# Kernel tuning notes

Hardware: AMD Instinct MI355X
Metric: run time of the kernel (lower is better)

## Reference

```python
import jax, jax.numpy as jnp
import numpy as np

GRID_SHAPE = (256, 256)  # SOM lattice dims -> M = 65536 nodes, ndim = 2
D = 32                   # input feature dim
B = 2048                 # batch size


def _make_grid_flat():
    # tf.meshgrid(indexing='ij') stacked on last axis, flattened to [1, M, ndim]
    mesh = np.stack(np.meshgrid(*[np.arange(s) for s in GRID_SHAPE], indexing='ij'), axis=-1)
    g = mesh.reshape(1, -1, len(GRID_SHAPE)).astype(np.float32)
    # faithful to source: per-axis mean (reduce_mean axis=1), GLOBAL std (reduce_std, no axis)
    g = (g - g.mean(axis=1, keepdims=True)) / g.std()
    return jnp.asarray(g)


def setup_inputs() -> dict:
    key = jax.random.key(0)
    k1, k2 = jax.random.split(key)
    grid_flat = _make_grid_flat()                                  # [1, M, 2]
    M = grid_flat.shape[1]
    w = jax.random.normal(k1, (1, M, D), dtype=jnp.float32)        # codebook (non-trainable in source)
    x = jax.random.normal(k2, (B, D), dtype=jnp.float32)
    return {"x": x, "grid_flat": grid_flat, "w": w}


def reference(x, grid_flat, w):
    # squared L2 distance from each input to every codebook vector.
    # computed here without materializing the [B, M, D] broadcast.
    wm = w[0]  # [M, D]
    d2 = (jnp.sum(x * x, axis=1, keepdims=True)
          - 2.0 * (x @ wm.T)
          + jnp.sum(wm * wm, axis=1)[None, :])  # [B, M]
    # source: top_k(-|d2|, k=1); d2 >= 0 so abs is identity, kept for fidelity
    _, idx = jax.lax.top_k(-jnp.abs(d2), 1)  # idx: [B, 1]
    bmu = grid_flat[0][idx[:, 0]]            # gather winning grid coords -> [B, 2]
    return bmu
```

## Files before the change

kernel.cpp:

```cpp
#include <hip/hip_runtime.h>
#include <stdint.h>

#define D       32
#define B       2048
#define M       65536
#define STRIPS  1024
#define CHUNKS  4
#define CHCOLS  (B / CHUNKS)
#define NTILES  (CHCOLS / 16)
#define SGROUPS 32
#define SPERG   (STRIPS / SGROUPS)

typedef _Float16 half8  __attribute__((ext_vector_type(8)));
typedef _Float16 half4v __attribute__((ext_vector_type(4)));
typedef float    floatx4 __attribute__((ext_vector_type(4)));


__device__ __forceinline__ uint32_t f32_sortable(float f) {
    uint32_t u = __float_as_uint(f);
    u ^= (uint32_t)((int32_t)u >> 31) | 0x80000000u;
    return u;
}

__global__ void som_prep_kernel(const float* __restrict__ x,
                                _Float16* __restrict__ xh,
                                _Float16* __restrict__ xl) {
    int i = (blockIdx.x * 256 + threadIdx.x) * 4;
    float4 v = *(const float4*)(x + i);
    half4v h, l;
    h[0] = (_Float16)v.x; l[0] = (_Float16)(v.x - (float)h[0]);
    h[1] = (_Float16)v.y; l[1] = (_Float16)(v.y - (float)h[1]);
    h[2] = (_Float16)v.z; l[2] = (_Float16)(v.z - (float)h[2]);
    h[3] = (_Float16)v.w; l[3] = (_Float16)(v.w - (float)h[3]);
    *(half4v*)(xh + i) = h;
    *(half4v*)(xl + i) = l;
}

__global__ __launch_bounds__(256, 4)
void som_mfma_kernel(const float* __restrict__ w,
                     const _Float16* __restrict__ x_hi,
                     const _Float16* __restrict__ x_lo,
                     uint32_t* __restrict__ pmax) {
    const int s    = blockIdx.x;
    const int wv   = threadIdx.x >> 6;
    const int lane = threadIdx.x & 63;
    const int q    = lane >> 4;
    const int j    = lane & 15;

    half8 a_hi[4], a_lo[4];
    float nrm[4];
#pragma unroll
    for (int t = 0; t < 4; t++) {
        const float* wp = w + (size_t)(s * 64 + t * 16 + j) * D + q * 8;
        float4 f0 = ((const float4*)wp)[0];
        float4 f1 = ((const float4*)wp)[1];
        float f[8] = {f0.x, f0.y, f0.z, f0.w, f1.x, f1.y, f1.z, f1.w};
        float sq = 0.0f;
#pragma unroll
        for (int k = 0; k < 8; k++) {
            _Float16 h = (_Float16)f[k];
            a_hi[t][k] = h;
            a_lo[t][k] = (_Float16)(f[k] - (float)h);
            sq = fmaf(f[k], f[k], sq);
        }
        sq += __shfl_xor(sq, 16);
        sq += __shfl_xor(sq, 32);
        nrm[t] = sq;
    }

    floatx4 init[4];
#pragma unroll
    for (int t = 0; t < 4; t++)
#pragma unroll
        for (int r = 0; r < 4; r++)
            init[t][r] = -0.5f * __shfl(nrm[t], q * 4 + r);

    uint32_t* pm = pmax + (size_t)s * B;

#pragma unroll 2
    for (int it = 0; it < NTILES; it++) {
        const int col = wv * CHCOLS + it * 16 + j;
        const half8 bh = *(const half8*)(x_hi + (size_t)col * D + q * 8);
        const half8 bl = *(const half8*)(x_lo + (size_t)col * D + q * 8);

        floatx4 acc[4];
#pragma unroll
        for (int t = 0; t < 4; t++)
            acc[t] = __builtin_amdgcn_mfma_f32_16x16x32_f16(a_lo[t], bh, init[t], 0, 0, 0);
#pragma unroll
        for (int t = 0; t < 4; t++)
            acc[t] = __builtin_amdgcn_mfma_f32_16x16x32_f16(a_hi[t], bl, acc[t], 0, 0, 0);
#pragma unroll
        for (int t = 0; t < 4; t++)
            acc[t] = __builtin_amdgcn_mfma_f32_16x16x32_f16(a_hi[t], bh, acc[t], 0, 0, 0);

        float b0 = fmaxf(fmaxf(acc[0][0], acc[0][1]), fmaxf(acc[0][2], acc[0][3]));
        float b1 = fmaxf(fmaxf(acc[1][0], acc[1][1]), fmaxf(acc[1][2], acc[1][3]));
        float b2 = fmaxf(fmaxf(acc[2][0], acc[2][1]), fmaxf(acc[2][2], acc[2][3]));
        float b3 = fmaxf(fmaxf(acc[3][0], acc[3][1]), fmaxf(acc[3][2], acc[3][3]));
        float best = fmaxf(fmaxf(b0, b1), fmaxf(b2, b3));

        best = fmaxf(best, __shfl_xor(best, 16));
        best = fmaxf(best, __shfl_xor(best, 32));

        if (lane < 16) pm[col] = f32_sortable(best);
    }
}

__global__ void som_reduce1_kernel(const uint32_t* __restrict__ pmax,
                                   uint64_t* __restrict__ s2) {
    const int col = blockIdx.x * 256 + threadIdx.x;
    const int sg  = blockIdx.y;
    uint32_t best = pmax[(size_t)(sg * SPERG) * B + col];
    int bstrip = sg * SPERG;
#pragma unroll 8
    for (int t = 1; t < SPERG; t++) {
        uint32_t u = pmax[(size_t)(sg * SPERG + t) * B + col];
        if (u > best) { best = u; bstrip = sg * SPERG + t; }
    }
    s2[(size_t)sg * B + col] = ((uint64_t)best << 32) | (uint32_t)(~(uint32_t)bstrip);
}

__global__ __launch_bounds__(256)
void som_final_kernel(const uint64_t* __restrict__ s2,
                      const float* __restrict__ x,
                      const float* __restrict__ w,
                      const float* __restrict__ grid_flat,
                      float* __restrict__ out) {
    const int wv   = threadIdx.x >> 6;
    const int lane = threadIdx.x & 63;
    const int col  = blockIdx.x * 4 + wv;

    uint64_t k = (lane < SGROUPS) ? s2[(size_t)lane * B + col] : 0ull;
    {
        uint64_t o;
        o = (uint64_t)__shfl_xor((long long)k,  1); if (o > k) k = o;
        o = (uint64_t)__shfl_xor((long long)k,  2); if (o > k) k = o;
        o = (uint64_t)__shfl_xor((long long)k,  4); if (o > k) k = o;
        o = (uint64_t)__shfl_xor((long long)k,  8); if (o > k) k = o;
        o = (uint64_t)__shfl_xor((long long)k, 16); if (o > k) k = o;
        o = (uint64_t)__shfl_xor((long long)k, 32); if (o > k) k = o;
    }
    const int strip = (int)(~(uint32_t)k);
    const int row   = strip * 64 + lane;

    const float* xc = x + (size_t)col * D;
    const float* wr = w + (size_t)row * D;
    float acc = 0.0f, nn = 0.0f;
#pragma unroll
    for (int i = 0; i < D; i++) {
        const float wv_ = wr[i];
        acc = fmaf(xc[i], wv_, acc);
        nn  = fmaf(wv_, wv_, nn);
    }
    const float score = acc - 0.5f * nn;

    uint64_t key = ((uint64_t)f32_sortable(score) << 32) | (uint32_t)(~(uint32_t)row);
    {
        uint64_t o;
        o = (uint64_t)__shfl_xor((long long)key,  1); if (o > key) key = o;
        o = (uint64_t)__shfl_xor((long long)key,  2); if (o > key) key = o;
        o = (uint64_t)__shfl_xor((long long)key,  4); if (o > key) key = o;
        o = (uint64_t)__shfl_xor((long long)key,  8); if (o > key) key = o;
        o = (uint64_t)__shfl_xor((long long)key, 16); if (o > key) key = o;
        o = (uint64_t)__shfl_xor((long long)key, 32); if (o > key) key = o;
    }
    if (lane == 0) {
        const uint32_t idx = ~(uint32_t)key;
        ((float2*)out)[col] = ((const float2*)grid_flat)[idx];
    }
}

#define MTILES  128
#define MTILE   (M / MTILES)
#define BTILE   256

__global__ void som_wnorm_kernel(const float* __restrict__ w,
                                 float* __restrict__ wnorm) {
    int t   = blockIdx.x * blockDim.x + threadIdx.x;
    int row = t >> 2;
    int j   = t & 3;
    const float4* p = (const float4*)(w + (size_t)row * D) + j * 2;
    float4 a = p[0];
    float4 b4 = p[1];
    float s = a.x * a.x + a.y * a.y + a.z * a.z + a.w * a.w
            + b4.x * b4.x + b4.y * b4.y + b4.z * b4.z + b4.w * b4.w;
    s += __shfl_xor(s, 1);
    s += __shfl_xor(s, 2);
    if (j == 0) wnorm[row] = 0.5f * s;
}

__global__ __launch_bounds__(BTILE, 8)
void som_score_kernel(const float* __restrict__ x,
                      const float* __restrict__ w,
                      const float* __restrict__ wnorm,
                      float* __restrict__ pscore,
                      int*   __restrict__ pidx) {
    const int bt = blockIdx.x;
    const int mt = blockIdx.y;
    const int b  = bt * BTILE + threadIdx.x;

    float xr[D];
    const float4* xp = (const float4*)(x + (size_t)b * D);
#pragma unroll
    for (int i = 0; i < D / 4; i++) {
        float4 v = xp[i];
        xr[4 * i + 0] = v.x; xr[4 * i + 1] = v.y;
        xr[4 * i + 2] = v.z; xr[4 * i + 3] = v.w;
    }

    const int m0 = mt * MTILE;
    float best = -3.0e38f;
    int   bidx = m0;
#pragma unroll 2
    for (int mm = 0; mm < MTILE; mm++) {
        const int m = m0 + mm;
        const float* __restrict__ wr = w + (size_t)m * D;
        float acc = 0.0f;
#pragma unroll
        for (int i = 0; i < D; i++) acc = fmaf(xr[i], wr[i], acc);
        const float score = acc - wnorm[m];
        if (score > best) { best = score; bidx = m; }
    }
    pscore[(size_t)b * MTILES + mt] = best;
    pidx  [(size_t)b * MTILES + mt] = bidx;
}

__global__ void som_reduce_kernel(const float* __restrict__ pscore,
                                  const int*   __restrict__ pidx,
                                  const float* __restrict__ grid_flat,
                                  float* __restrict__ out) {
    const int b = blockIdx.x * blockDim.x + threadIdx.x;
    const float* ps = pscore + (size_t)b * MTILES;
    const int*   pi = pidx   + (size_t)b * MTILES;
    float best = -3.0e38f;
    int   bidx = 0x7fffffff;
#pragma unroll 4
    for (int t = 0; t < MTILES; t++) {
        const float s  = ps[t];
        const int   id = pi[t];
        if (s > best || (s == best && id < bidx)) { best = s; bidx = id; }
    }
    ((float2*)out)[b] = ((const float2*)grid_flat)[bidx];
}

extern "C" void kernel_launch(void* const* d_in, const int* in_sizes, int n_in,
                              void* d_out, int out_size, void* d_ws, size_t ws_size,
                              hipStream_t stream) {
    const float* x         = (const float*)d_in[0];
    const float* grid_flat = (const float*)d_in[1];
    const float* w         = (const float*)d_in[2];
    float* out = (float*)d_out;

    char* ws = (char*)d_ws;
    const size_t XH_OFF = 0;
    const size_t XL_OFF = XH_OFF + (size_t)B * D * sizeof(_Float16);
    const size_t PM_OFF = XL_OFF + (size_t)B * D * sizeof(_Float16);
    const size_t S2_OFF = PM_OFF + (size_t)STRIPS * B * sizeof(uint32_t);
    const size_t NEED   = S2_OFF + (size_t)SGROUPS * B * sizeof(uint64_t);

    if (ws_size >= NEED) {
        _Float16* x_hi = (_Float16*)(ws + XH_OFF);
        _Float16* x_lo = (_Float16*)(ws + XL_OFF);
        uint32_t* pmax = (uint32_t*)(ws + PM_OFF);
        uint64_t* s2   = (uint64_t*)(ws + S2_OFF);

        som_prep_kernel<<<(B * D / 4) / 256, 256, 0, stream>>>(x, x_hi, x_lo);
        som_mfma_kernel<<<STRIPS, 256, 0, stream>>>(w, x_hi, x_lo, pmax);
        som_reduce1_kernel<<<dim3(B / 256, SGROUPS), 256, 0, stream>>>(pmax, s2);
        som_final_kernel<<<B / 4, 256, 0, stream>>>(s2, x, w, grid_flat, out);
    } else {
        float* wnorm  = (float*)d_ws;
        float* pscore = wnorm + M;
        int*   pidx   = (int*)(pscore + (size_t)B * MTILES);

        som_wnorm_kernel<<<(M * 4) / 256, 256, 0, stream>>>(w, wnorm);
        dim3 grid1(B / BTILE, MTILES);
        som_score_kernel<<<grid1, BTILE, 0, stream>>>(x, w, wnorm, pscore, pidx);
        som_reduce_kernel<<<B / 256, 256, 0, stream>>>(pscore, pidx, grid_flat, out);
    }
}
```

Before: 99.94 us.

## Screen with single fp16 MFMA, then exactly rescore top candidate strips within margin

Replaces the split hi/lo fp16 three-MFMA emulation of fp32 with a single fp16 MFMA pass that only screens strips, then picks the top-3 strips per column and rescores in fp32 every strip whose screened score lies within a fixed margin of the best. This cuts MFMA work and the x_lo prep/load by about two thirds. It also replaces the two-stage strip reduction with a per-column top-3 selection kernel. Correctness now relies on the fp16 error staying below the fixed margin, and inputs that produce many near-ties make the fallback scan and rescoring expensive.

```diff
diff --git a/kernel.cpp b/kernel.cpp
--- a/kernel.cpp
+++ b/kernel.cpp
@@ -8,8 +8,7 @@
 #define CHUNKS  4
 #define CHCOLS  (B / CHUNKS)
 #define NTILES  (CHCOLS / 16)
-#define SGROUPS 32
-#define SPERG   (STRIPS / SGROUPS)
+#define MARGIN  0.15f
 
 typedef _Float16 half8  __attribute__((ext_vector_type(8)));
 typedef _Float16 half4v __attribute__((ext_vector_type(4)));
@@ -21,33 +20,32 @@
     u ^= (uint32_t)((int32_t)u >> 31) | 0x80000000u;
     return u;
 }
+__device__ __forceinline__ float sort_decode(uint32_t u) {
+    uint32_t m = (u & 0x80000000u) ? (u ^ 0x80000000u) : ~u;
+    return __uint_as_float(m);
+}
 
 __global__ void som_prep_kernel(const float* __restrict__ x,
-                                _Float16* __restrict__ xh,
-                                _Float16* __restrict__ xl) {
+                                _Float16* __restrict__ xh) {
     int i = (blockIdx.x * 256 + threadIdx.x) * 4;
     float4 v = *(const float4*)(x + i);
-    half4v h, l;
-    h[0] = (_Float16)v.x; l[0] = (_Float16)(v.x - (float)h[0]);
-    h[1] = (_Float16)v.y; l[1] = (_Float16)(v.y - (float)h[1]);
-    h[2] = (_Float16)v.z; l[2] = (_Float16)(v.z - (float)h[2]);
-    h[3] = (_Float16)v.w; l[3] = (_Float16)(v.w - (float)h[3]);
+    half4v h;
+    h[0] = (_Float16)v.x; h[1] = (_Float16)v.y;
+    h[2] = (_Float16)v.z; h[3] = (_Float16)v.w;
     *(half4v*)(xh + i) = h;
-    *(half4v*)(xl + i) = l;
 }
 
 __global__ __launch_bounds__(256, 4)
-void som_mfma_kernel(const float* __restrict__ w,
-                     const _Float16* __restrict__ x_hi,
-                     const _Float16* __restrict__ x_lo,
-                     uint32_t* __restrict__ pmax) {
+void som_screen_kernel(const float* __restrict__ w,
+                       const _Float16* __restrict__ x_hi,
+                       uint32_t* __restrict__ pmax) {
     const int s    = blockIdx.x;
     const int wv   = threadIdx.x >> 6;
     const int lane = threadIdx.x & 63;
     const int q    = lane >> 4;
     const int j    = lane & 15;
 
-    half8 a_hi[4], a_lo[4];
+    half8 a_hi[4];
     float nrm[4];
 #pragma unroll
     for (int t = 0; t < 4; t++) {
@@ -58,9 +56,7 @@
         float sq = 0.0f;
 #pragma unroll
         for (int k = 0; k < 8; k++) {
-            _Float16 h = (_Float16)f[k];
-            a_hi[t][k] = h;
-            a_lo[t][k] = (_Float16)(f[k] - (float)h);
+            a_hi[t][k] = (_Float16)f[k];
             sq = fmaf(f[k], f[k], sq);
         }
         sq += __shfl_xor(sq, 16);
@@ -81,18 +77,11 @@
     for (int it = 0; it < NTILES; it++) {
         const int col = wv * CHCOLS + it * 16 + j;
         const half8 bh = *(const half8*)(x_hi + (size_t)col * D + q * 8);
-        const half8 bl = *(const half8*)(x_lo + (size_t)col * D + q * 8);
 
         floatx4 acc[4];
 #pragma unroll
         for (int t = 0; t < 4; t++)
-            acc[t] = __builtin_amdgcn_mfma_f32_16x16x32_f16(a_lo[t], bh, init[t], 0, 0, 0);
-#pragma unroll
-        for (int t = 0; t < 4; t++)
-            acc[t] = __builtin_amdgcn_mfma_f32_16x16x32_f16(a_hi[t], bl, acc[t], 0, 0, 0);
-#pragma unroll
-        for (int t = 0; t < 4; t++)
-            acc[t] = __builtin_amdgcn_mfma_f32_16x16x32_f16(a_hi[t], bh, acc[t], 0, 0, 0);
+            acc[t] = __builtin_amdgcn_mfma_f32_16x16x32_f16(a_hi[t], bh, init[t], 0, 0, 0);
 
         float b0 = fmaxf(fmaxf(acc[0][0], acc[0][1]), fmaxf(acc[0][2], acc[0][3]));
         float b1 = fmaxf(fmaxf(acc[1][0], acc[1][1]), fmaxf(acc[1][2], acc[1][3]));
@@ -107,22 +96,87 @@
     }
 }
 
-__global__ void som_reduce1_kernel(const uint32_t* __restrict__ pmax,
-                                   uint64_t* __restrict__ s2) {
-    const int col = blockIdx.x * 256 + threadIdx.x;
-    const int sg  = blockIdx.y;
-    uint32_t best = pmax[(size_t)(sg * SPERG) * B + col];
-    int bstrip = sg * SPERG;
-#pragma unroll 8
-    for (int t = 1; t < SPERG; t++) {
-        uint32_t u = pmax[(size_t)(sg * SPERG + t) * B + col];
-        if (u > best) { best = u; bstrip = sg * SPERG + t; }
-    }
-    s2[(size_t)sg * B + col] = ((uint64_t)best << 32) | (uint32_t)(~(uint32_t)bstrip);
+__device__ __forceinline__ void top3_insert(uint64_t& k0, uint64_t& k1,
+                                            uint64_t& k2, uint64_t k) {
+    if (k > k2) {
+        if (k > k1) {
+            k2 = k1;
+            if (k > k0) { k1 = k0; k0 = k; } else { k1 = k; }
+        } else {
+            k2 = k;
+        }
+    }
 }
 
 __global__ __launch_bounds__(256)
-void som_final_kernel(const uint64_t* __restrict__ s2,
+void som_select_kernel(const uint32_t* __restrict__ pmax,
+                       uint64_t* __restrict__ cand) {
+    __shared__ uint64_t lk[256 * 3];
+    const int c  = threadIdx.x & 31;
+    const int sg = threadIdx.x >> 5;
+    const int col = blockIdx.x * 32 + c;
+
+    uint64_t k0 = 0, k1 = 0, k2 = 0;
+    for (int i = 0; i < 128; i++) {
+        const int strip = sg * 128 + i;
+        const uint32_t u = pmax[(size_t)strip * B + col];
+        const uint64_t k = ((uint64_t)u << 32) | (uint32_t)(~(uint32_t)strip);
+        top3_insert(k0, k1, k2, k);
+    }
+    lk[threadIdx.x * 3 + 0] = k0;
+    lk[threadIdx.x * 3 + 1] = k1;
+    lk[threadIdx.x * 3 + 2] = k2;
+    __syncthreads();
+
+    if (threadIdx.x < 32) {
+        uint64_t m0 = 0, m1 = 0, m2 = 0;
+#pragma unroll
+        for (int sgi = 0; sgi < 8; sgi++) {
+            const int t = sgi * 32 + threadIdx.x;
+            top3_insert(m0, m1, m2, lk[t * 3 + 0]);
+            top3_insert(m0, m1, m2, lk[t * 3 + 1]);
+            top3_insert(m0, m1, m2, lk[t * 3 + 2]);
+        }
+        const int gcol = blockIdx.x * 32 + threadIdx.x;
+        cand[(size_t)gcol * 3 + 0] = m0;
+        cand[(size_t)gcol * 3 + 1] = m1;
+        cand[(size_t)gcol * 3 + 2] = m2;
+    }
+}
+
+__device__ __forceinline__ void rescore_strip(int strip, int lane,
+                                              const float* __restrict__ w,
+                                              const float* xr,
+                                              uint64_t& best) {
+    const int row = strip * 64 + lane;
+    const float* wr = w + (size_t)row * D;
+    float4 w0 = ((const float4*)wr)[0];
+    float4 w1 = ((const float4*)wr)[1];
+    float4 w2 = ((const float4*)wr)[2];
+    float4 w3 = ((const float4*)wr)[3];
+    float4 w4 = ((const float4*)wr)[4];
+    float4 w5 = ((const float4*)wr)[5];
+    float4 w6 = ((const float4*)wr)[6];
+    float4 w7 = ((const float4*)wr)[7];
+    const float wf[32] = {w0.x,w0.y,w0.z,w0.w, w1.x,w1.y,w1.z,w1.w,
+                          w2.x,w2.y,w2.z,w2.w, w3.x,w3.y,w3.z,w3.w,
+                          w4.x,w4.y,w4.z,w4.w, w5.x,w5.y,w5.z,w5.w,
+                          w6.x,w6.y,w6.z,w6.w, w7.x,w7.y,w7.z,w7.w};
+    float acc = 0.0f, nn = 0.0f;
+#pragma unroll
+    for (int i = 0; i < D; i++) {
+        acc = fmaf(xr[i], wf[i], acc);
+        nn  = fmaf(wf[i], wf[i], nn);
+    }
+    const float score = acc - 0.5f * nn;
+    const uint64_t key = ((uint64_t)f32_sortable(score) << 32)
+                       | (uint32_t)(~(uint32_t)row);
+    if (key > best) best = key;
+}
+
+__global__ __launch_bounds__(256)
+void som_final_kernel(const uint64_t* __restrict__ cand,
+                      const uint32_t* __restrict__ pmax,
                       const float* __restrict__ x,
                       const float* __restrict__ w,
                       const float* __restrict__ grid_flat,
@@ -131,42 +185,53 @@
     const int lane = threadIdx.x & 63;
     const int col  = blockIdx.x * 4 + wv;
 
-    uint64_t k = (lane < SGROUPS) ? s2[(size_t)lane * B + col] : 0ull;
+    const uint64_t c0 = cand[(size_t)col * 3 + 0];
+    const uint64_t c1 = cand[(size_t)col * 3 + 1];
+    const uint64_t c2 = cand[(size_t)col * 3 + 2];
+    const int s1 = (int)(~(uint32_t)c0);
+    const int s2 = (int)(~(uint32_t)c1);
+    const float v1 = sort_decode((uint32_t)(c0 >> 32));
+    const float v2 = sort_decode((uint32_t)(c1 >> 32));
+    const float v3 = sort_decode((uint32_t)(c2 >> 32));
+    const float thresh = v1 - MARGIN;
+
+    float xr[D];
+    const float4* xp = (const float4*)(x + (size_t)col * D);
+#pragma unroll
+    for (int i = 0; i < D / 4; i++) {
+        float4 v = xp[i];
+        xr[4*i+0] = v.x; xr[4*i+1] = v.y; xr[4*i+2] = v.z; xr[4*i+3] = v.w;
+    }
+
+    uint64_t best = 0;
+    rescore_strip(s1, lane, w, xr, best);
+    if (v2 >= thresh) rescore_strip(s2, lane, w, xr, best);
+    if (v3 >= thresh) {
+        for (int t = 0; t < STRIPS / 64; t++) {
+            const int strip_l = lane + t * 64;
+            const uint32_t u = pmax[(size_t)strip_l * B + col];
+            const bool qual = (sort_decode(u) >= thresh)
+                              && strip_l != s1 && strip_l != s2;
+            unsigned long long mask = __ballot(qual);
+            while (mask) {
+                const int ln = __ffsll(mask) - 1;
+                mask &= mask - 1;
+                rescore_strip(ln + t * 64, lane, w, xr, best);
+            }
+        }
+    }
+
     {
         uint64_t o;
-        o = (uint64_t)__shfl_xor((long long)k,  1); if (o > k) k = o;
-        o = (uint64_t)__shfl_xor((long long)k,  2); if (o > k) k = o;
-        o = (uint64_t)__shfl_xor((long long)k,  4); if (o > k) k = o;
-        o = (uint64_t)__shfl_xor((long long)k,  8); if (o > k) k = o;
-        o = (uint64_t)__shfl_xor((long long)k, 16); if (o > k) k = o;
-        o = (uint64_t)__shfl_xor((long long)k, 32); if (o > k) k = o;
-    }
-    const int strip = (int)(~(uint32_t)k);
-    const int row   = strip * 64 + lane;
-
-    const float* xc = x + (size_t)col * D;
-    const float* wr = w + (size_t)row * D;
-    float acc = 0.0f, nn = 0.0f;
-#pragma unroll
-    for (int i = 0; i < D; i++) {
-        const float wv_ = wr[i];
-        acc = fmaf(xc[i], wv_, acc);
-        nn  = fmaf(wv_, wv_, nn);
-    }
-    const float score = acc - 0.5f * nn;
-
-    uint64_t key = ((uint64_t)f32_sortable(score) << 32) | (uint32_t)(~(uint32_t)row);
-    {
-        uint64_t o;
-        o = (uint64_t)__shfl_xor((long long)key,  1); if (o > key) key = o;
-        o = (uint64_t)__shfl_xor((long long)key,  2); if (o > key) key = o;
-        o = (uint64_t)__shfl_xor((long long)key,  4); if (o > key) key = o;
-        o = (uint64_t)__shfl_xor((long long)key,  8); if (o > key) key = o;
-        o = (uint64_t)__shfl_xor((long long)key, 16); if (o > key) key = o;
-        o = (uint64_t)__shfl_xor((long long)key, 32); if (o > key) key = o;
+        o = (uint64_t)__shfl_xor((long long)best,  1); if (o > best) best = o;
+        o = (uint64_t)__shfl_xor((long long)best,  2); if (o > best) best = o;
+        o = (uint64_t)__shfl_xor((long long)best,  4); if (o > best) best = o;
+        o = (uint64_t)__shfl_xor((long long)best,  8); if (o > best) best = o;
+        o = (uint64_t)__shfl_xor((long long)best, 16); if (o > best) best = o;
+        o = (uint64_t)__shfl_xor((long long)best, 32); if (o > best) best = o;
     }
     if (lane == 0) {
-        const uint32_t idx = ~(uint32_t)key;
+        const uint32_t idx = ~(uint32_t)best;
         ((float2*)out)[col] = ((const float2*)grid_flat)[idx];
     }
 }
@@ -254,21 +319,19 @@
 
     char* ws = (char*)d_ws;
     const size_t XH_OFF = 0;
-    const size_t XL_OFF = XH_OFF + (size_t)B * D * sizeof(_Float16);
-    const size_t PM_OFF = XL_OFF + (size_t)B * D * sizeof(_Float16);
-    const size_t S2_OFF = PM_OFF + (size_t)STRIPS * B * sizeof(uint32_t);
-    const size_t NEED   = S2_OFF + (size_t)SGROUPS * B * sizeof(uint64_t);
+    const size_t PM_OFF = XH_OFF + (size_t)B * D * sizeof(_Float16);
+    const size_t CD_OFF = PM_OFF + (size_t)STRIPS * B * sizeof(uint32_t);
+    const size_t NEED   = CD_OFF + (size_t)B * 3 * sizeof(uint64_t);
 
     if (ws_size >= NEED) {
         _Float16* x_hi = (_Float16*)(ws + XH_OFF);
-        _Float16* x_lo = (_Float16*)(ws + XL_OFF);
         uint32_t* pmax = (uint32_t*)(ws + PM_OFF);
-        uint64_t* s2   = (uint64_t*)(ws + S2_OFF);
-
-        som_prep_kernel<<<(B * D / 4) / 256, 256, 0, stream>>>(x, x_hi, x_lo);
-        som_mfma_kernel<<<STRIPS, 256, 0, stream>>>(w, x_hi, x_lo, pmax);
-        som_reduce1_kernel<<<dim3(B / 256, SGROUPS), 256, 0, stream>>>(pmax, s2);
-        som_final_kernel<<<B / 4, 256, 0, stream>>>(s2, x, w, grid_flat, out);
+        uint64_t* cand = (uint64_t*)(ws + CD_OFF);
+
+        som_prep_kernel<<<(B * D / 4) / 256, 256, 0, stream>>>(x, x_hi);
+        som_screen_kernel<<<STRIPS, 256, 0, stream>>>(w, x_hi, pmax);
+        som_select_kernel<<<B / 32, 256, 0, stream>>>(pmax, cand);
+        som_final_kernel<<<B / 4, 256, 0, stream>>>(cand, pmax, x, w, grid_flat, out);
     } else {
         float* wnorm  = (float*)d_ws;
         float* pscore = wnorm + M;
```

Result: slower. 178.6 us (+78.7%).
